# Kernel optimization log

Measured on AMD Instinct MI355X. Metric: run time of the kernel, lower is better.

Reference implementation:

```python
import jax, jax.numpy as jnp
import numpy as np

N, D, BS = 262144, 64, 12  # nodes, eigvec dim, graphs per batch


def setup_inputs() -> dict:
    key = jax.random.key(0)
    k1, k2, k3 = jax.random.split(key, 3)
    inp = jax.random.normal(k1, (N, D), dtype=jnp.float32)
    tgt = jax.random.normal(k2, (N, D), dtype=jnp.float32)
    batch = jnp.sort(jax.random.randint(k3, (N,), 0, BS)).astype(jnp.int64)
    return {"input": inp, "target": tgt, "batch": batch, "batch_size": BS}


def _sign_combinations(batch_size, dtype):
    # itertools.product([1, -1], repeat=batch_size): first row all +1, last all -1.
    idx = jnp.arange(2 ** batch_size)
    shifts = (batch_size - 1) - jnp.arange(batch_size)
    bits = (idx[:, None] >> shifts[None, :]) & 1  # 0 -> +1, 1 -> -1
    return (1 - 2 * bits).astype(dtype)  # [2^BS, BS]


def reference(input, target, batch, batch_size):
    combos = _sign_combinations(batch_size, input.dtype)  # [C, BS]
    # Per-combination loss sum((s*x - t)^2) = sum(x^2) + sum(t^2) - 2 * sum_g s_g * e_g
    # where e_g = sum over nodes in graph g of <x_i, t_i>. Same math, no [C, N, D] blowup.
    cross = jax.ops.segment_sum(jnp.sum(input * target, axis=1), batch,
                                num_segments=batch_size)  # [BS]
    const = jnp.sum(input * input) + jnp.sum(target * target)
    combined_loss = const - 2.0 * (combos @ cross)  # [C]
    loss_idx = jnp.argmin(combined_loss)
    signed = combos[loss_idx][batch][:, None]  # [N, 1]
    loss = jnp.sum((input * signed - target) ** 2)  # F.mse_loss reduction='sum'
    return loss
```

## Files before the change

### kernel.cpp

```cpp
#include <hip/hip_runtime.h>

#define NBINS 12
#define GRID1 2048
#define BLK 256

__global__ __launch_bounds__(BLK) void umse_partial(
    const float4* __restrict__ x4, const float4* __restrict__ t4,
    const int* __restrict__ batch32, float* __restrict__ blockOut,
    int nNodes)
{
    __shared__ float cross_lds[NBINS];
    __shared__ float wsum[BLK / 64];
    __shared__ int s_is64;

    const int tid = threadIdx.x;
    if (tid < NBINS) cross_lds[tid] = 0.0f;
    if (tid == 0) {
        s_is64 = (batch32[nNodes - 1] == 0) ? 1 : 0;
    }
    __syncthreads();
    const int is64 = s_is64;

    const long total  = (long)nNodes * 16;
    const long stride = (long)GRID1 * BLK;
    long idx = (long)blockIdx.x * BLK + tid;
    const long iters = (total + stride - 1) / stride;

    float sumsq = 0.0f;
    const int lane = tid & 63;

    for (long it = 0; it < iters; ++it, idx += stride) {
        float p = 0.0f;
        if (idx < total) {
            float4 a = x4[idx];
            float4 b = t4[idx];
            p = a.x * b.x + a.y * b.y + a.z * b.z + a.w * b.w;
            sumsq += a.x * a.x + a.y * a.y + a.z * a.z + a.w * a.w
                   + b.x * b.x + b.y * b.y + b.z * b.z + b.w * b.w;
        }
        p += __shfl_xor(p, 1);
        p += __shfl_xor(p, 2);
        p += __shfl_xor(p, 4);
        p += __shfl_xor(p, 8);
        if ((lane & 15) == 0 && idx < total) {
            long node = idx >> 4;
            int g = is64 ? batch32[(int)(node << 1)] : batch32[(int)node];
            atomicAdd(&cross_lds[g], p);
        }
    }

    __syncthreads();

    for (int m = 32; m; m >>= 1) sumsq += __shfl_xor(sumsq, m);
    const int wid = tid >> 6;
    if (lane == 0) wsum[wid] = sumsq;
    __syncthreads();

    float* dst = blockOut + (long)blockIdx.x * 16;
    if (tid == 0) {
        float s = 0.0f;
        for (int w = 0; w < BLK / 64; ++w) s += wsum[w];
        dst[12] = s;
    }
    if (tid < NBINS) dst[tid] = cross_lds[tid];
}

__global__ __launch_bounds__(BLK) void umse_final(
    const float* __restrict__ blockOut, float* __restrict__ out, int G)
{
    __shared__ double cols[16];
    const int tid = threadIdx.x;
    const int wid = tid >> 6, lane = tid & 63;

    for (int c = wid; c < 13; c += 4) {
        double s = 0.0;
        for (int b = lane; b < G; b += 64) s += (double)blockOut[(long)b * 16 + c];
        for (int m = 32; m; m >>= 1) s += __shfl_xor(s, m);
        if (lane == 0) cols[c] = s;
    }
    __syncthreads();

    if (tid == 0) {
        double sum = cols[12];
        double acc = 0.0;
        for (int g = 0; g < NBINS; ++g) acc += fabs(cols[g]);
        out[0] = (float)(sum - 2.0 * acc);
    }
}

extern "C" void kernel_launch(void* const* d_in, const int* in_sizes, int n_in,
                              void* d_out, int out_size, void* d_ws, size_t ws_size,
                              hipStream_t stream)
{
    const float* x = (const float*)d_in[0];
    const float* t = (const float*)d_in[1];
    const int* batch = (const int*)d_in[2];
    const int nNodes = in_sizes[2];
    float* ws = (float*)d_ws;
    float* out = (float*)d_out;

    umse_partial<<<GRID1, BLK, 0, stream>>>(
        (const float4*)x, (const float4*)t, batch, ws, nNodes);
    umse_final<<<1, BLK, 0, stream>>>(ws, out, GRID1);
}
```

Baseline: 170.2 us.

## Use contiguous per-block chunks with run-length group accumulation to cut LDS atomics

Each block now takes a contiguous chunk of the node data instead of grid-striding. Each thread keeps a running per-graph accumulator, exploiting sorted batch ids, so the shuffle reduction and LDS atomic only happen when the group changes rather than on every iteration. A template specialization drops bounds checks when sizes divide evenly, and the workspace is transposed so the final kernel reduces each of the 13 columns with one wave of an 832-thread block. The FULL path assumes all 16 lanes of a node group change group in lockstep, and contiguous chunks change the coalescing pattern across blocks.

```diff
diff --git a/kernel.cpp b/kernel.cpp
--- a/kernel.cpp
+++ b/kernel.cpp
@@ -4,10 +4,18 @@
 #define GRID1 2048
 #define BLK 256
 
+__device__ __forceinline__ void flush_group(float acc, int g, float* cross_lds, int lane) {
+    acc += __shfl_xor(acc, 1);
+    acc += __shfl_xor(acc, 2);
+    acc += __shfl_xor(acc, 4);
+    acc += __shfl_xor(acc, 8);
+    if ((lane & 15) == 0) atomicAdd(&cross_lds[g], acc);
+}
+
+template <bool FULL>
 __global__ __launch_bounds__(BLK) void umse_partial(
     const float4* __restrict__ x4, const float4* __restrict__ t4,
-    const int* __restrict__ batch32, float* __restrict__ blockOut,
-    int nNodes)
+    const int* __restrict__ batch32, float* __restrict__ ws, int nNodes)
 {
     __shared__ float cross_lds[NBINS];
     __shared__ float wsum[BLK / 64];
@@ -20,71 +28,86 @@
     }
     __syncthreads();
     const int is64 = s_is64;
+    const int lane = tid & 63;
 
-    const long total  = (long)nNodes * 16;
-    const long stride = (long)GRID1 * BLK;
-    long idx = (long)blockIdx.x * BLK + tid;
-    const long iters = (total + stride - 1) / stride;
+    const int total = nNodes * 16;
+    const int per_block = (total + GRID1 - 1) / GRID1;
+    const int start = blockIdx.x * per_block;
+    const int end = min(start + per_block, total);
 
     float sumsq = 0.0f;
-    const int lane = tid & 63;
+    float acc = 0.0f;
+    int curg = -1;
 
-    for (long it = 0; it < iters; ++it, idx += stride) {
-        float p = 0.0f;
-        if (idx < total) {
+    if (FULL) {
+        for (int idx = start + tid; idx < end; idx += BLK) {
             float4 a = x4[idx];
             float4 b = t4[idx];
-            p = a.x * b.x + a.y * b.y + a.z * b.z + a.w * b.w;
-            sumsq += a.x * a.x + a.y * a.y + a.z * a.z + a.w * a.w
-                   + b.x * b.x + b.y * b.y + b.z * b.z + b.w * b.w;
+            int node = idx >> 4;
+            int g = is64 ? batch32[node << 1] : batch32[node];
+            sumsq += a.x*a.x + a.y*a.y + a.z*a.z + a.w*a.w
+                   + b.x*b.x + b.y*b.y + b.z*b.z + b.w*b.w;
+            float p = a.x*b.x + a.y*b.y + a.z*b.z + a.w*b.w;
+            if (g != curg) {
+                if (curg >= 0) flush_group(acc, curg, cross_lds, lane);
+                curg = g;
+                acc = p;
+            } else {
+                acc += p;
+            }
         }
-        p += __shfl_xor(p, 1);
-        p += __shfl_xor(p, 2);
-        p += __shfl_xor(p, 4);
-        p += __shfl_xor(p, 8);
-        if ((lane & 15) == 0 && idx < total) {
-            long node = idx >> 4;
-            int g = is64 ? batch32[(int)(node << 1)] : batch32[(int)node];
-            atomicAdd(&cross_lds[g], p);
+        if (curg >= 0) flush_group(acc, curg, cross_lds, lane);
+    } else {
+        for (int base = start; base < end; base += BLK) {
+            int idx = base + tid;
+            if (idx >= end) continue;
+            float4 a = x4[idx];
+            float4 b = t4[idx];
+            int node = idx >> 4;
+            int g = is64 ? batch32[node << 1] : batch32[node];
+            sumsq += a.x*a.x + a.y*a.y + a.z*a.z + a.w*a.w
+                   + b.x*b.x + b.y*b.y + b.z*b.z + b.w*b.w;
+            float p = a.x*b.x + a.y*b.y + a.z*b.z + a.w*b.w;
+            if (g != curg) {
+                if (curg >= 0) atomicAdd(&cross_lds[curg], acc);
+                curg = g;
+                acc = p;
+            } else {
+                acc += p;
+            }
         }
+        if (curg >= 0) atomicAdd(&cross_lds[curg], acc);
     }
 
+    for (int m = 32; m; m >>= 1) sumsq += __shfl_xor(sumsq, m);
+    if (lane == 0) wsum[tid >> 6] = sumsq;
     __syncthreads();
 
-    for (int m = 32; m; m >>= 1) sumsq += __shfl_xor(sumsq, m);
-    const int wid = tid >> 6;
-    if (lane == 0) wsum[wid] = sumsq;
-    __syncthreads();
-
-    float* dst = blockOut + (long)blockIdx.x * 16;
     if (tid == 0) {
         float s = 0.0f;
         for (int w = 0; w < BLK / 64; ++w) s += wsum[w];
-        dst[12] = s;
+        ws[12 * GRID1 + blockIdx.x] = s;
     }
-    if (tid < NBINS) dst[tid] = cross_lds[tid];
+    if (tid < NBINS) ws[tid * GRID1 + blockIdx.x] = cross_lds[tid];
 }
 
-__global__ __launch_bounds__(BLK) void umse_final(
-    const float* __restrict__ blockOut, float* __restrict__ out, int G)
+__global__ __launch_bounds__(832) void umse_final(
+    const float* __restrict__ ws, float* __restrict__ out)
 {
-    __shared__ double cols[16];
+    __shared__ double cols[13];
     const int tid = threadIdx.x;
-    const int wid = tid >> 6, lane = tid & 63;
+    const int w = tid >> 6, lane = tid & 63;
 
-    for (int c = wid; c < 13; c += 4) {
-        double s = 0.0;
-        for (int b = lane; b < G; b += 64) s += (double)blockOut[(long)b * 16 + c];
-        for (int m = 32; m; m >>= 1) s += __shfl_xor(s, m);
-        if (lane == 0) cols[c] = s;
-    }
+    double s = 0.0;
+    for (int b = lane; b < GRID1; b += 64) s += (double)ws[w * GRID1 + b];
+    for (int m = 32; m; m >>= 1) s += __shfl_xor(s, m);
+    if (lane == 0) cols[w] = s;
     __syncthreads();
 
     if (tid == 0) {
-        double sum = cols[12];
         double acc = 0.0;
         for (int g = 0; g < NBINS; ++g) acc += fabs(cols[g]);
-        out[0] = (float)(sum - 2.0 * acc);
+        out[0] = (float)(cols[12] - 2.0 * acc);
     }
 }
 
@@ -99,7 +122,16 @@
     float* ws = (float*)d_ws;
     float* out = (float*)d_out;
 
-    umse_partial<<<GRID1, BLK, 0, stream>>>(
-        (const float4*)x, (const float4*)t, batch, ws, nNodes);
-    umse_final<<<1, BLK, 0, stream>>>(ws, out, GRID1);
+    const long total = (long)nNodes * 16;
+    const int per_block = (int)((total + GRID1 - 1) / GRID1);
+    const bool full = (total % GRID1 == 0) && (per_block % BLK == 0);
+
+    if (full) {
+        umse_partial<true><<<GRID1, BLK, 0, stream>>>(
+            (const float4*)x, (const float4*)t, batch, ws, nNodes);
+    } else {
+        umse_partial<false><<<GRID1, BLK, 0, stream>>>(
+            (const float4*)x, (const float4*)t, batch, ws, nNodes);
+    }
+    umse_final<<<1, 832, 0, stream>>>(ws, out);
 }
```

Result: faster. 160.8 us (-5.5%).

## Fuse partial and final reductions with last-block-done counter and contiguous per-block chunks

Applied to the files above, without the earlier changes.

Merges the two-kernel reduction into one kernel. Global atomics accumulate the 12 graph bins and the sum of squares, and a completion counter lets the last block compute the output. Each block now reads a contiguous chunk, and when the whole chunk falls in one graph it skips the per-node batch lookups and LDS atomics. The cost is an extra memset launch, global atomic contention across blocks, and float rather than double accumulation in the final sum.

```diff
diff --git a/kernel.cpp b/kernel.cpp
--- a/kernel.cpp
+++ b/kernel.cpp
@@ -4,87 +4,109 @@
 #define GRID1 2048
 #define BLK 256
 
-__global__ __launch_bounds__(BLK) void umse_partial(
+__global__ __launch_bounds__(BLK) void umse_fused(
     const float4* __restrict__ x4, const float4* __restrict__ t4,
-    const int* __restrict__ batch32, float* __restrict__ blockOut,
-    int nNodes)
+    const int* __restrict__ batch32,
+    float* __restrict__ bins, unsigned int* __restrict__ counter,
+    float* __restrict__ out, int nNodes)
 {
     __shared__ float cross_lds[NBINS];
-    __shared__ float wsum[BLK / 64];
-    __shared__ int s_is64;
+    __shared__ float redA[BLK / 64], redB[BLK / 64];
+    __shared__ int s_info[3];
+    __shared__ unsigned s_done;
+    __shared__ float fbins[13];
 
     const int tid = threadIdx.x;
+    const int lane = tid & 63;
+    const int wid = tid >> 6;
+
+    const int total = nNodes * 16;
+    const int per_block = (total + GRID1 - 1) / GRID1;
+    const int start = blockIdx.x * per_block;
+    const int end = min(start + per_block, total);
+
+    if (tid == 0) {
+        int is64 = (batch32[nNodes - 1] == 0) ? 1 : 0;
+        int n0 = start >> 4;
+        int n1 = (end - 1) >> 4;
+        s_info[0] = is64;
+        s_info[1] = is64 ? batch32[n0 << 1] : batch32[n0];
+        s_info[2] = is64 ? batch32[n1 << 1] : batch32[n1];
+    }
     if (tid < NBINS) cross_lds[tid] = 0.0f;
-    if (tid == 0) {
-        s_is64 = (batch32[nNodes - 1] == 0) ? 1 : 0;
-    }
     __syncthreads();
-    const int is64 = s_is64;
-
-    const long total  = (long)nNodes * 16;
-    const long stride = (long)GRID1 * BLK;
-    long idx = (long)blockIdx.x * BLK + tid;
-    const long iters = (total + stride - 1) / stride;
+    const int is64 = s_info[0];
+    const int gfirst = s_info[1], glast = s_info[2];
 
     float sumsq = 0.0f;
-    const int lane = tid & 63;
+    float dot = 0.0f;
 
-    for (long it = 0; it < iters; ++it, idx += stride) {
-        float p = 0.0f;
-        if (idx < total) {
+    const bool fast = (gfirst == glast) && (end - start == 8 * BLK);
+
+    if (fast) {
+        const float4* xa = x4 + start + tid;
+        const float4* ta = t4 + start + tid;
+        #pragma unroll
+        for (int k = 0; k < 8; ++k) {
+            float4 a = xa[k * BLK];
+            float4 b = ta[k * BLK];
+            sumsq += a.x * a.x + a.y * a.y + a.z * a.z + a.w * a.w
+                   + b.x * b.x + b.y * b.y + b.z * b.z + b.w * b.w;
+            dot   += a.x * b.x + a.y * b.y + a.z * b.z + a.w * b.w;
+        }
+    } else {
+        float acc = 0.0f;
+        int curg = -1;
+        for (int idx = start + tid; idx < end; idx += BLK) {
             float4 a = x4[idx];
             float4 b = t4[idx];
-            p = a.x * b.x + a.y * b.y + a.z * b.z + a.w * b.w;
+            int node = idx >> 4;
+            int g = is64 ? batch32[node << 1] : batch32[node];
             sumsq += a.x * a.x + a.y * a.y + a.z * a.z + a.w * a.w
                    + b.x * b.x + b.y * b.y + b.z * b.z + b.w * b.w;
+            float p = a.x * b.x + a.y * b.y + a.z * b.z + a.w * b.w;
+            if (g != curg) {
+                if (curg >= 0) atomicAdd(&cross_lds[curg], acc);
+                curg = g;
+                acc = p;
+            } else {
+                acc += p;
+            }
         }
-        p += __shfl_xor(p, 1);
-        p += __shfl_xor(p, 2);
-        p += __shfl_xor(p, 4);
-        p += __shfl_xor(p, 8);
-        if ((lane & 15) == 0 && idx < total) {
-            long node = idx >> 4;
-            int g = is64 ? batch32[(int)(node << 1)] : batch32[(int)node];
-            atomicAdd(&cross_lds[g], p);
-        }
+        if (curg >= 0) atomicAdd(&cross_lds[curg], acc);
     }
 
-    __syncthreads();
-
-    for (int m = 32; m; m >>= 1) sumsq += __shfl_xor(sumsq, m);
-    const int wid = tid >> 6;
-    if (lane == 0) wsum[wid] = sumsq;
-    __syncthreads();
-
-    float* dst = blockOut + (long)blockIdx.x * 16;
-    if (tid == 0) {
-        float s = 0.0f;
-        for (int w = 0; w < BLK / 64; ++w) s += wsum[w];
-        dst[12] = s;
+    for (int m = 32; m; m >>= 1) {
+        sumsq += __shfl_xor(sumsq, m);
+        dot   += __shfl_xor(dot, m);
     }
-    if (tid < NBINS) dst[tid] = cross_lds[tid];
-}
-
-__global__ __launch_bounds__(BLK) void umse_final(
-    const float* __restrict__ blockOut, float* __restrict__ out, int G)
-{
-    __shared__ double cols[16];
-    const int tid = threadIdx.x;
-    const int wid = tid >> 6, lane = tid & 63;
-
-    for (int c = wid; c < 13; c += 4) {
-        double s = 0.0;
-        for (int b = lane; b < G; b += 64) s += (double)blockOut[(long)b * 16 + c];
-        for (int m = 32; m; m >>= 1) s += __shfl_xor(s, m);
-        if (lane == 0) cols[c] = s;
-    }
+    if (lane == 0) { redA[wid] = sumsq; redB[wid] = dot; }
     __syncthreads();
 
     if (tid == 0) {
-        double sum = cols[12];
-        double acc = 0.0;
-        for (int g = 0; g < NBINS; ++g) acc += fabs(cols[g]);
-        out[0] = (float)(sum - 2.0 * acc);
+        atomicAdd(&bins[12], redA[0] + redA[1] + redA[2] + redA[3]);
+        if (fast)
+            atomicAdd(&bins[gfirst], redB[0] + redB[1] + redB[2] + redB[3]);
+    }
+    if (!fast && tid < NBINS) {
+        float v = cross_lds[tid];
+        if (v != 0.0f) atomicAdd(&bins[tid], v);
+    }
+
+    __threadfence();
+    if (tid == 0) s_done = atomicAdd(counter, 1u);
+    __syncthreads();
+    if (s_done == GRID1 - 1) {
+        __threadfence();
+        if (tid < 13)
+            fbins[tid] = __hip_atomic_load(&bins[tid], __ATOMIC_RELAXED,
+                                           __HIP_MEMORY_SCOPE_AGENT);
+        __syncthreads();
+        if (tid == 0) {
+            float acc = 0.0f;
+            for (int g = 0; g < NBINS; ++g) acc += fabsf(fbins[g]);
+            out[0] = fbins[12] - 2.0f * acc;
+        }
     }
 }
 
@@ -96,10 +118,11 @@
     const float* t = (const float*)d_in[1];
     const int* batch = (const int*)d_in[2];
     const int nNodes = in_sizes[2];
-    float* ws = (float*)d_ws;
+    float* bins = (float*)d_ws;
+    unsigned int* counter = (unsigned int*)((float*)d_ws + 13);
     float* out = (float*)d_out;
 
-    umse_partial<<<GRID1, BLK, 0, stream>>>(
-        (const float4*)x, (const float4*)t, batch, ws, nNodes);
-    umse_final<<<1, BLK, 0, stream>>>(ws, out, GRID1);
+    hipMemsetAsync(d_ws, 0, 64, stream);
+    umse_fused<<<GRID1, BLK, 0, stream>>>(
+        (const float4*)x, (const float4*)t, batch, bins, counter, out, nNodes);
 }
```

After: 475.6 us. +179.4%, slower.

## Unroll streaming loop by two with nontemporal loads and transpose partials layout

Applied to the files above, without the earlier changes.

The main loop is unrolled by two so each thread keeps four independent float4 loads in flight, and it uses nontemporal loads with 32-bit indexing. Full iterations run without bounds checks, and a single guarded remainder step handles the leftover elements. Per-block partials are now stored column-major, so the final kernel can give each of its 13 wavefronts one contiguous column to reduce. The aim is more memory-level parallelism and less per-iteration overhead in a bandwidth-bound reduction, at the cost of relying on 32-bit index arithmetic fitting the problem size.

```diff
diff --git a/kernel.cpp b/kernel.cpp
--- a/kernel.cpp
+++ b/kernel.cpp
@@ -3,88 +3,104 @@
 #define NBINS 12
 #define GRID1 2048
 #define BLK 256
+#define STRIDE (GRID1 * BLK)
+
+typedef float f4 __attribute__((ext_vector_type(4)));
+
+__device__ __forceinline__ float dot4(f4 a, f4 b) {
+    return a.x * b.x + a.y * b.y + a.z * b.z + a.w * b.w;
+}
+__device__ __forceinline__ float sq4(f4 a) {
+    return a.x * a.x + a.y * a.y + a.z * a.z + a.w * a.w;
+}
+__device__ __forceinline__ void red16_atomic(float p, int g, float* cross, int lane) {
+    p += __shfl_xor(p, 1);
+    p += __shfl_xor(p, 2);
+    p += __shfl_xor(p, 4);
+    p += __shfl_xor(p, 8);
+    if ((lane & 15) == 0) atomicAdd(&cross[g], p);
+}
 
 __global__ __launch_bounds__(BLK) void umse_partial(
-    const float4* __restrict__ x4, const float4* __restrict__ t4,
-    const int* __restrict__ batch32, float* __restrict__ blockOut,
-    int nNodes)
+    const f4* __restrict__ x4, const f4* __restrict__ t4,
+    const int* __restrict__ batch32, float* __restrict__ ws, int nNodes)
 {
     __shared__ float cross_lds[NBINS];
-    __shared__ float wsum[BLK / 64];
-    __shared__ int s_is64;
+    __shared__ float redA[BLK / 64];
 
     const int tid = threadIdx.x;
-    if (tid < NBINS) cross_lds[tid] = 0.0f;
-    if (tid == 0) {
-        s_is64 = (batch32[nNodes - 1] == 0) ? 1 : 0;
-    }
-    __syncthreads();
-    const int is64 = s_is64;
-
-    const long total  = (long)nNodes * 16;
-    const long stride = (long)GRID1 * BLK;
-    long idx = (long)blockIdx.x * BLK + tid;
-    const long iters = (total + stride - 1) / stride;
-
-    float sumsq = 0.0f;
     const int lane = tid & 63;
 
-    for (long it = 0; it < iters; ++it, idx += stride) {
-        float p = 0.0f;
-        if (idx < total) {
-            float4 a = x4[idx];
-            float4 b = t4[idx];
-            p = a.x * b.x + a.y * b.y + a.z * b.z + a.w * b.w;
-            sumsq += a.x * a.x + a.y * a.y + a.z * a.z + a.w * a.w
-                   + b.x * b.x + b.y * b.y + b.z * b.z + b.w * b.w;
-        }
-        p += __shfl_xor(p, 1);
-        p += __shfl_xor(p, 2);
-        p += __shfl_xor(p, 4);
-        p += __shfl_xor(p, 8);
-        if ((lane & 15) == 0 && idx < total) {
-            long node = idx >> 4;
-            int g = is64 ? batch32[(int)(node << 1)] : batch32[(int)node];
-            atomicAdd(&cross_lds[g], p);
-        }
+    if (tid < NBINS) cross_lds[tid] = 0.0f;
+    const int is64 = (batch32[nNodes - 1] == 0) ? 1 : 0;
+    __syncthreads();
+
+    const int total = nNodes * 16;
+    const int nIter = total / STRIDE;
+    float sumsq = 0.0f;
+    int idx = blockIdx.x * BLK + tid;
+
+    int it = 0;
+    for (; it + 1 < nIter; it += 2, idx += 2 * STRIDE) {
+        const int i0 = idx, i1 = idx + STRIDE;
+        f4 a0 = __builtin_nontemporal_load(x4 + i0);
+        f4 b0 = __builtin_nontemporal_load(t4 + i0);
+        f4 a1 = __builtin_nontemporal_load(x4 + i1);
+        f4 b1 = __builtin_nontemporal_load(t4 + i1);
+        const int n0 = i0 >> 4, n1 = i1 >> 4;
+        const int g0 = is64 ? batch32[n0 << 1] : batch32[n0];
+        const int g1 = is64 ? batch32[n1 << 1] : batch32[n1];
+        sumsq += sq4(a0) + sq4(b0) + sq4(a1) + sq4(b1);
+        red16_atomic(dot4(a0, b0), g0, cross_lds, lane);
+        red16_atomic(dot4(a1, b1), g1, cross_lds, lane);
+    }
+    for (; it < nIter; ++it, idx += STRIDE) {
+        f4 a = __builtin_nontemporal_load(x4 + idx);
+        f4 b = __builtin_nontemporal_load(t4 + idx);
+        const int n = idx >> 4;
+        const int g = is64 ? batch32[n << 1] : batch32[n];
+        sumsq += sq4(a) + sq4(b);
+        red16_atomic(dot4(a, b), g, cross_lds, lane);
+    }
+    if (idx < total) {
+        f4 a = x4[idx];
+        f4 b = t4[idx];
+        const int n = idx >> 4;
+        const int g = is64 ? batch32[n << 1] : batch32[n];
+        sumsq += sq4(a) + sq4(b);
+        atomicAdd(&cross_lds[g], dot4(a, b));
     }
 
+    for (int m = 32; m; m >>= 1) sumsq += __shfl_xor(sumsq, m);
+    if (lane == 0) redA[tid >> 6] = sumsq;
     __syncthreads();
 
-    for (int m = 32; m; m >>= 1) sumsq += __shfl_xor(sumsq, m);
-    const int wid = tid >> 6;
-    if (lane == 0) wsum[wid] = sumsq;
-    __syncthreads();
-
-    float* dst = blockOut + (long)blockIdx.x * 16;
-    if (tid == 0) {
+    if (tid < NBINS) ws[tid * GRID1 + blockIdx.x] = cross_lds[tid];
+    if (tid == NBINS) {
         float s = 0.0f;
-        for (int w = 0; w < BLK / 64; ++w) s += wsum[w];
-        dst[12] = s;
+        #pragma unroll
+        for (int w = 0; w < BLK / 64; ++w) s += redA[w];
+        ws[NBINS * GRID1 + blockIdx.x] = s;
     }
-    if (tid < NBINS) dst[tid] = cross_lds[tid];
 }
 
-__global__ __launch_bounds__(BLK) void umse_final(
-    const float* __restrict__ blockOut, float* __restrict__ out, int G)
+__global__ __launch_bounds__(832) void umse_final(
+    const float* __restrict__ ws, float* __restrict__ out)
 {
-    __shared__ double cols[16];
+    __shared__ double cols[13];
     const int tid = threadIdx.x;
-    const int wid = tid >> 6, lane = tid & 63;
+    const int w = tid >> 6, lane = tid & 63;
 
-    for (int c = wid; c < 13; c += 4) {
-        double s = 0.0;
-        for (int b = lane; b < G; b += 64) s += (double)blockOut[(long)b * 16 + c];
-        for (int m = 32; m; m >>= 1) s += __shfl_xor(s, m);
-        if (lane == 0) cols[c] = s;
-    }
+    double s = 0.0;
+    for (int b = lane; b < GRID1; b += 64) s += (double)ws[w * GRID1 + b];
+    for (int m = 32; m; m >>= 1) s += __shfl_xor(s, m);
+    if (lane == 0) cols[w] = s;
     __syncthreads();
 
     if (tid == 0) {
-        double sum = cols[12];
         double acc = 0.0;
         for (int g = 0; g < NBINS; ++g) acc += fabs(cols[g]);
-        out[0] = (float)(sum - 2.0 * acc);
+        out[0] = (float)(cols[12] - 2.0 * acc);
     }
 }
 
@@ -100,6 +116,6 @@
     float* out = (float*)d_out;
 
     umse_partial<<<GRID1, BLK, 0, stream>>>(
-        (const float4*)x, (const float4*)t, batch, ws, nNodes);
-    umse_final<<<1, BLK, 0, stream>>>(ws, out, GRID1);
+        (const f4*)x, (const f4*)t, batch, ws, nNodes);
+    umse_final<<<1, 832, 0, stream>>>(ws, out);
 }
```

New measurement: 156.0 us. -8.4%, faster.
